# Kernel optimization log

Measured on AMD Instinct MI355X. Metric: run time of the kernel, lower is better.

Reference implementation:

```python
import jax, jax.numpy as jnp
import numpy as np

N = 100000   # nodes
E = 1600000  # edges (avg degree 16)
IN_DIM = 5
HID = 128
OUT_DIM = 1


def gcn_conv(x, src, dst, W, b, n):
    """PyG GCNConv: out = D^{-1/2}(A+I)D^{-1/2} (x @ W) + b, self-loops added."""
    h = x @ W  # [N, F_out]
    # degree including self-loop (edge weight 1 each)
    deg = jax.ops.segment_sum(jnp.ones(src.shape[0], h.dtype), dst, num_segments=n) + 1.0
    dinv = jax.lax.rsqrt(deg)  # deg >= 1 always (self-loop)
    coef = dinv[src] * dinv[dst]  # [E]
    agg = jax.ops.segment_sum(h[src] * coef[:, None], dst, num_segments=n)
    agg = agg + h * (dinv * dinv)[:, None]  # self-loop contribution
    return agg + b


def setup_inputs() -> dict:
    key = jax.random.key(0)
    k = jax.random.split(key, 6)
    x = jax.random.normal(k[0], (N, IN_DIM), jnp.float32)
    edge_index = jax.random.randint(k[1], (2, E), 0, N)
    W1 = jax.random.normal(k[2], (IN_DIM, HID), jnp.float32) / np.float32(np.sqrt(IN_DIM))
    b1 = jnp.zeros((HID,), jnp.float32)
    W2 = jax.random.normal(k[3], (HID, OUT_DIM), jnp.float32) / np.float32(np.sqrt(HID))
    b2 = jnp.zeros((OUT_DIM,), jnp.float32)
    return {"x": x, "edge_index": edge_index, "W1": W1, "b1": b1, "W2": W2, "b2": b2}


def reference(x, edge_index, W1, b1, W2, b2):
    src, dst = edge_index[0], edge_index[1]
    h = gcn_conv(x, src, dst, W1, b1, N)
    h = jax.nn.relu(h)
    out = gcn_conv(h, src, dst, W2, b2, N)
    return out
```

## Files before the change

### kernel.cpp

```cpp
#include <hip/hip_runtime.h>
#include <hip/hip_fp16.h>

#define Nn 100000
#define Ee 1600000
#define HID 128
#define IN_DIM 5

#define SH 10
#define BSZ 1024
#define NB 98
#define BCAP 18432

#define PCHUNK 4000
#define PBLK (Ee / PCHUNK)

typedef float f32x4 __attribute__((ext_vector_type(4)));
union F2H { float f; __half2 h; };

__global__ void zero_kernel(int* __restrict__ bcnt) {
    if (threadIdx.x < NB) bcnt[threadIdx.x] = 0;
}

__global__ __launch_bounds__(512) void partition_kernel(const int* __restrict__ src,
                                                        const int* __restrict__ dst,
                                                        unsigned int* __restrict__ recs,
                                                        int* __restrict__ bcnt) {
    __shared__ unsigned int stage[PCHUNK];
    __shared__ int hist[NB + 1];
    __shared__ int cur[NB];
    __shared__ int gbase[NB];
    int e0 = blockIdx.x * PCHUNK;
    if (threadIdx.x <= NB) hist[threadIdx.x] = 0;
    __syncthreads();
    for (int e = e0 + threadIdx.x; e < e0 + PCHUNK; e += 512)
        atomicAdd(&hist[(dst[e] >> SH) + 1], 1);
    __syncthreads();
    if (threadIdx.x == 0)
        for (int b = 1; b <= NB; ++b) hist[b] += hist[b - 1];
    __syncthreads();
    if (threadIdx.x < NB) {
        int c0 = hist[threadIdx.x], c1 = hist[threadIdx.x + 1];
        cur[threadIdx.x] = c0;
        gbase[threadIdx.x] = atomicAdd(&bcnt[threadIdx.x], c1 - c0);
    }
    __syncthreads();
    for (int e = e0 + threadIdx.x; e < e0 + PCHUNK; e += 512) {
        int d = dst[e], s = src[e];
        int b = d >> SH;
        int slot = atomicAdd(&cur[b], 1);
        stage[slot] = ((unsigned int)(d & (BSZ - 1)) << 17) | (unsigned int)s;
    }
    __syncthreads();
    int wave = threadIdx.x >> 6, lane = threadIdx.x & 63;
    for (int b = wave; b < NB; b += 8) {
        int c0 = hist[b], len = hist[b + 1] - c0;
        unsigned int* o = recs + (size_t)b * BCAP + gbase[b];
        for (int i = lane; i < len; i += 64) o[i] = stage[c0 + i];
    }
}

__global__ __launch_bounds__(1024) void sortk_kernel(const unsigned int* __restrict__ recs,
                                                     const int* __restrict__ bcnt,
                                                     const float* __restrict__ x,
                                                     int* __restrict__ degc,
                                                     unsigned int* __restrict__ nodeoff,
                                                     unsigned int* __restrict__ ssrc,
                                                     float* __restrict__ dinv,
                                                     f32x4* __restrict__ xd16) {
    __shared__ int cnt[BSZ];
    __shared__ int scanbuf[BSZ];
    __shared__ int cur[BSZ];
    int b = blockIdx.x, tid = threadIdx.x;
    int n = bcnt[b];
    cnt[tid] = 0;
    __syncthreads();
    const unsigned int* R = recs + (size_t)b * BCAP;
    for (int i = tid; i < n; i += 1024)
        atomicAdd(&cnt[R[i] >> 17], 1);
    __syncthreads();
    int v = cnt[tid];
    scanbuf[tid] = v;
    __syncthreads();
    for (int ofs = 1; ofs < BSZ; ofs <<= 1) {
        int t = (tid >= ofs) ? scanbuf[tid - ofs] : 0;
        __syncthreads();
        scanbuf[tid] += t;
        __syncthreads();
    }
    int excl = scanbuf[tid] - v;
    cur[tid] = excl;
    int g = (b << SH) + tid;
    if (g < Nn) {
        degc[g] = v;
        nodeoff[g] = (unsigned int)(b * BCAP + excl);
        float di = rsqrtf((float)v + 1.0f);
        dinv[g] = di;
        f32x4 o;
        o.x = x[g * IN_DIM + 0] * di;
        o.y = x[g * IN_DIM + 1] * di;
        o.z = x[g * IN_DIM + 2] * di;
        F2H u;
        u.h = __floats2half2_rn(x[g * IN_DIM + 3] * di, x[g * IN_DIM + 4] * di);
        o.w = u.f;
        xd16[g] = o;
    }
    __syncthreads();
    unsigned int* O = ssrc + (size_t)b * BCAP;
    for (int i = tid; i < n; i += 1024) {
        unsigned int r = R[i];
        int pos = atomicAdd(&cur[r >> 17], 1);
        O[pos] = r & 0x1FFFFu;
    }
}

__global__ __launch_bounds__(256) void gcn1_kernel(const unsigned int* __restrict__ ssrc,
                                                   const unsigned int* __restrict__ nodeoff,
                                                   const int* __restrict__ degc,
                                                   const f32x4* __restrict__ xd16,
                                                   const float* __restrict__ dinv,
                                                   const float* __restrict__ W1,
                                                   const float* __restrict__ b1,
                                                   const float* __restrict__ W2,
                                                   float* __restrict__ h2d) {
    __shared__ float w1s[IN_DIM * HID];
    __shared__ float w2s[HID], b1s[HID];
    int tid = threadIdx.x;
    for (int j = tid; j < IN_DIM * HID; j += 256) w1s[j] = W1[j];
    if (tid < HID) { w2s[tid] = W2[tid]; b1s[tid] = b1[tid]; }
    __syncthreads();
    int nd = blockIdx.x * 256 + tid;
    if (nd >= Nn) return;
    unsigned int off = nodeoff[nd];
    int len = degc[nd];
    float a0 = 0.f, a1 = 0.f, a2 = 0.f, a3 = 0.f, a4 = 0.f;
    int i = 0;
    for (; i + 4 <= len; i += 4) {
        unsigned int s0 = ssrc[off + i], s1 = ssrc[off + i + 1];
        unsigned int s2 = ssrc[off + i + 2], s3 = ssrc[off + i + 3];
        f32x4 v0 = xd16[s0], v1 = xd16[s1], v2 = xd16[s2], v3 = xd16[s3];
        F2H u0, u1, u2, u3;
        u0.f = v0.w; u1.f = v1.w; u2.f = v2.w; u3.f = v3.w;
        float2 e0 = __half22float2(u0.h), e1 = __half22float2(u1.h);
        float2 e2 = __half22float2(u2.h), e3 = __half22float2(u3.h);
        a0 += (v0.x + v1.x) + (v2.x + v3.x);
        a1 += (v0.y + v1.y) + (v2.y + v3.y);
        a2 += (v0.z + v1.z) + (v2.z + v3.z);
        a3 += (e0.x + e1.x) + (e2.x + e3.x);
        a4 += (e0.y + e1.y) + (e2.y + e3.y);
    }
    for (; i < len; ++i) {
        unsigned int s = ssrc[off + i];
        f32x4 v = xd16[s];
        F2H u; u.f = v.w; float2 e = __half22float2(u.h);
        a0 += v.x; a1 += v.y; a2 += v.z; a3 += e.x; a4 += e.y;
    }
    float di = dinv[nd];
    f32x4 sv = xd16[nd];
    F2H su; su.f = sv.w; float2 se = __half22float2(su.h);
    a0 = (a0 + sv.x) * di;
    a1 = (a1 + sv.y) * di;
    a2 = (a2 + sv.z) * di;
    a3 = (a3 + se.x) * di;
    a4 = (a4 + se.y) * di;
    float accp = 0.f;
    #pragma unroll
    for (int f = 0; f < HID; ++f) {
        float v = b1s[f] + a0 * w1s[f] + a1 * w1s[HID + f] + a2 * w1s[2 * HID + f]
                + a3 * w1s[3 * HID + f] + a4 * w1s[4 * HID + f];
        accp += fmaxf(v, 0.f) * w2s[f];
    }
    h2d[nd] = accp * di;
}

__global__ __launch_bounds__(256) void gcn2_kernel(const unsigned int* __restrict__ ssrc,
                                                   const unsigned int* __restrict__ nodeoff,
                                                   const int* __restrict__ degc,
                                                   const float* __restrict__ h2d,
                                                   const float* __restrict__ dinv,
                                                   const float* __restrict__ b2,
                                                   float* __restrict__ out) {
    int nd = blockIdx.x * 256 + threadIdx.x;
    if (nd >= Nn) return;
    unsigned int off = nodeoff[nd];
    int len = degc[nd];
    float s = 0.f;
    int i = 0;
    for (; i + 8 <= len; i += 8) {
        float t0 = h2d[ssrc[off + i]],     t1 = h2d[ssrc[off + i + 1]];
        float t2 = h2d[ssrc[off + i + 2]], t3 = h2d[ssrc[off + i + 3]];
        float t4 = h2d[ssrc[off + i + 4]], t5 = h2d[ssrc[off + i + 5]];
        float t6 = h2d[ssrc[off + i + 6]], t7 = h2d[ssrc[off + i + 7]];
        s += ((t0 + t1) + (t2 + t3)) + ((t4 + t5) + (t6 + t7));
    }
    for (; i < len; ++i) s += h2d[ssrc[off + i]];
    out[nd] = (s + h2d[nd]) * dinv[nd] + b2[0];
}

extern "C" void kernel_launch(void* const* d_in, const int* in_sizes, int n_in,
                              void* d_out, int out_size, void* d_ws, size_t ws_size,
                              hipStream_t stream) {
    const float* x  = (const float*)d_in[0];
    const int*   ei = (const int*)d_in[1];
    const float* W1 = (const float*)d_in[2];
    const float* b1 = (const float*)d_in[3];
    const float* W2 = (const float*)d_in[4];
    const float* b2 = (const float*)d_in[5];
    const int* src = ei;
    const int* dst = ei + Ee;
    float* out = (float*)d_out;

    float* dinv = (float*)d_ws;
    f32x4* xd16 = (f32x4*)(dinv + Nn);
    float* h2d  = (float*)(xd16 + Nn);
    int* degc   = (int*)(h2d + Nn);
    unsigned int* nodeoff = (unsigned int*)(degc + Nn);
    unsigned int* recs = nodeoff + Nn;
    unsigned int* ssrc = recs + (size_t)NB * BCAP;
    int* bcnt = (int*)(ssrc + (size_t)NB * BCAP);

    zero_kernel<<<1, 128, 0, stream>>>(bcnt);
    partition_kernel<<<PBLK, 512, 0, stream>>>(src, dst, recs, bcnt);
    sortk_kernel<<<NB, 1024, 0, stream>>>(recs, bcnt, x, degc, nodeoff, ssrc, dinv, xd16);
    gcn1_kernel<<<(Nn + 255) / 256, 256, 0, stream>>>(ssrc, nodeoff, degc, xd16, dinv,
                                                      W1, b1, W2, h2d);
    gcn2_kernel<<<(Nn + 255) / 256, 256, 0, stream>>>(ssrc, nodeoff, degc, h2d, dinv, b2, out);
}
```

Before: 77.77 us.

## Shrink sort buckets to 256 nodes and use a wave-shuffle prefix scan

Bucket granularity drops from 1024 to 256 nodes, so the per-bucket sort kernel launches 391 blocks of 256 threads instead of 98 blocks of 1024, aiming to spread the sort across more compute units. The block-wide scan built on shared memory and many barriers becomes a wavefront shuffle scan followed by a small sum across waves. In exchange, the partition kernel must handle a 391-entry histogram: thread 0 runs a longer serial prefix, each block does more global atomics, and writes become smaller and more scattered per bucket. Bucket capacity is reduced to match.

```diff
diff --git a/kernel.cpp b/kernel.cpp
--- a/kernel.cpp
+++ b/kernel.cpp
@@ -6,10 +6,10 @@
 #define HID 128
 #define IN_DIM 5
 
-#define SH 10
-#define BSZ 1024
-#define NB 98
-#define BCAP 18432
+#define SH 8
+#define BSZ 256
+#define NB 391
+#define BCAP 4608
 
 #define PCHUNK 4000
 #define PBLK (Ee / PCHUNK)
@@ -30,7 +30,7 @@
     __shared__ int cur[NB];
     __shared__ int gbase[NB];
     int e0 = blockIdx.x * PCHUNK;
-    if (threadIdx.x <= NB) hist[threadIdx.x] = 0;
+    for (int i = threadIdx.x; i <= NB; i += 512) hist[i] = 0;
     __syncthreads();
     for (int e = e0 + threadIdx.x; e < e0 + PCHUNK; e += 512)
         atomicAdd(&hist[(dst[e] >> SH) + 1], 1);
@@ -59,35 +59,40 @@
     }
 }
 
-__global__ __launch_bounds__(1024) void sortk_kernel(const unsigned int* __restrict__ recs,
-                                                     const int* __restrict__ bcnt,
-                                                     const float* __restrict__ x,
-                                                     int* __restrict__ degc,
-                                                     unsigned int* __restrict__ nodeoff,
-                                                     unsigned int* __restrict__ ssrc,
-                                                     float* __restrict__ dinv,
-                                                     f32x4* __restrict__ xd16) {
+__global__ __launch_bounds__(BSZ) void sortk_kernel(const unsigned int* __restrict__ recs,
+                                                    const int* __restrict__ bcnt,
+                                                    const float* __restrict__ x,
+                                                    int* __restrict__ degc,
+                                                    unsigned int* __restrict__ nodeoff,
+                                                    unsigned int* __restrict__ ssrc,
+                                                    float* __restrict__ dinv,
+                                                    f32x4* __restrict__ xd16) {
     __shared__ int cnt[BSZ];
-    __shared__ int scanbuf[BSZ];
     __shared__ int cur[BSZ];
+    __shared__ int wsum[BSZ / 64];
     int b = blockIdx.x, tid = threadIdx.x;
     int n = bcnt[b];
     cnt[tid] = 0;
     __syncthreads();
     const unsigned int* R = recs + (size_t)b * BCAP;
-    for (int i = tid; i < n; i += 1024)
+    for (int i = tid; i < n; i += BSZ)
         atomicAdd(&cnt[R[i] >> 17], 1);
     __syncthreads();
     int v = cnt[tid];
-    scanbuf[tid] = v;
-    __syncthreads();
-    for (int ofs = 1; ofs < BSZ; ofs <<= 1) {
-        int t = (tid >= ofs) ? scanbuf[tid - ofs] : 0;
-        __syncthreads();
-        scanbuf[tid] += t;
-        __syncthreads();
-    }
-    int excl = scanbuf[tid] - v;
+    int lane = tid & 63, wid = tid >> 6;
+    int sc = v;
+    #pragma unroll
+    for (int ofs = 1; ofs < 64; ofs <<= 1) {
+        int t = __shfl_up(sc, ofs, 64);
+        if (lane >= ofs) sc += t;
+    }
+    if (lane == 63) wsum[wid] = sc;
+    __syncthreads();
+    int wpre = 0;
+    #pragma unroll
+    for (int w = 0; w < BSZ / 64; ++w)
+        if (w < wid) wpre += wsum[w];
+    int excl = wpre + sc - v;
     cur[tid] = excl;
     int g = (b << SH) + tid;
     if (g < Nn) {
@@ -106,7 +111,7 @@
     }
     __syncthreads();
     unsigned int* O = ssrc + (size_t)b * BCAP;
-    for (int i = tid; i < n; i += 1024) {
+    for (int i = tid; i < n; i += BSZ) {
         unsigned int r = R[i];
         int pos = atomicAdd(&cur[r >> 17], 1);
         O[pos] = r & 0x1FFFFu;
@@ -218,9 +223,9 @@
     unsigned int* ssrc = recs + (size_t)NB * BCAP;
     int* bcnt = (int*)(ssrc + (size_t)NB * BCAP);
 
-    zero_kernel<<<1, 128, 0, stream>>>(bcnt);
+    zero_kernel<<<1, 512, 0, stream>>>(bcnt);
     partition_kernel<<<PBLK, 512, 0, stream>>>(src, dst, recs, bcnt);
-    sortk_kernel<<<NB, 1024, 0, stream>>>(recs, bcnt, x, degc, nodeoff, ssrc, dinv, xd16);
+    sortk_kernel<<<NB, BSZ, 0, stream>>>(recs, bcnt, x, degc, nodeoff, ssrc, dinv, xd16);
     gcn1_kernel<<<(Nn + 255) / 256, 256, 0, stream>>>(ssrc, nodeoff, degc, xd16, dinv,
                                                       W1, b1, W2, h2d);
     gcn2_kernel<<<(Nn + 255) / 256, 256, 0, stream>>>(ssrc, nodeoff, degc, h2d, dinv, b2, out);
```

Result: slower. 81.87 us (+5.3%).
